# Performance work log

Hardware: AMD Instinct MI355X
Metric: run time of the kernel (lower is better)

The kernel has to match this reference:

```python
import jax, jax.numpy as jnp
import numpy as np

N = 100000   # nodes
E = 1600000  # edges (avg degree 16)
N_IN, N_HID, N_OUT = 64, 64, 16


def setup_inputs() -> dict:
    key = jax.random.key(0)
    k1, k2, k3, k4 = jax.random.split(key, 4)
    x = jax.random.normal(k1, (N, N_IN), dtype=jnp.float32)
    edge_index = jax.random.randint(k2, (2, E), 0, N, dtype=jnp.int64)
    # Glorot-style init like PyG GCNConv linear weights
    W1 = jax.random.normal(k3, (N_IN, N_HID), dtype=jnp.float32) * (1.0 / np.sqrt(N_IN))
    b1 = jnp.zeros((N_HID,), dtype=jnp.float32)
    W2 = jax.random.normal(k4, (N_HID, N_OUT), dtype=jnp.float32) * (1.0 / np.sqrt(N_HID))
    b2 = jnp.zeros((N_OUT,), dtype=jnp.float32)
    return {"x": x, "edge_index": edge_index, "W1": W1, "b1": b1, "W2": W2, "b2": b2}


def reference(x, edge_index, W1, b1, W2, b2):
    n = x.shape[0]
    # GCNConv default: add self-loops with weight 1, symmetric normalization
    loop = jnp.arange(n, dtype=edge_index.dtype)
    src = jnp.concatenate([edge_index[0], loop])  # [E+N]
    dst = jnp.concatenate([edge_index[1], loop])  # [E+N]
    w = jnp.ones(src.shape[0], dtype=x.dtype)
    deg = jax.ops.segment_sum(w, dst, num_segments=n)           # in-degree incl. self-loop
    dinv = jnp.where(deg > 0, jax.lax.rsqrt(deg), 0.0)
    norm = dinv[src] * w * dinv[dst]                            # [E+N] edge coefficients

    def gcn_conv(h, Wm, bm):
        h = h @ Wm                                              # [N, d_out] linear first (PyG order)
        msg = h[src] * norm[:, None]                            # gather + scale
        return jax.ops.segment_sum(msg, dst, num_segments=n) + bm  # scatter-add + bias

    h = jax.nn.relu(gcn_conv(x, W1, b1))
    # dropout is identity at inference (training=False)
    return jax.nn.log_softmax(gcn_conv(h, W2, b2), axis=1)
```

## Files before the change

### kernel.cpp

```cpp
#include <hip/hip_runtime.h>

constexpr int FIN = 64;
constexpr int FH  = 64;
constexpr int FO  = 16;


constexpr int BSH      = 7;
constexpr int BW       = 1 << BSH;
constexpr int NBUCK    = 1024;
constexpr int EPB_HIST = 16384;
constexpr int EPB_BIN  = 4096;

__device__ inline unsigned short f2bf(float f) {
    unsigned u = __float_as_uint(f);
    return (unsigned short)((u + 0x7FFFu + ((u >> 16) & 1u)) >> 16);
}
__device__ inline float bf2f(unsigned short h) {
    return __uint_as_float((unsigned)h << 16);
}
__device__ inline float4 bf4_to_f4(ushort4 u) {
    float4 f;
    f.x = bf2f(u.x); f.y = bf2f(u.y); f.z = bf2f(u.z); f.w = bf2f(u.w);
    return f;
}

__launch_bounds__(256)
__global__ void hist_kernel(const int* __restrict__ ei, int E, int* __restrict__ bcnt) {
    __shared__ int lh[NBUCK];
    int t = threadIdx.x;
    for (int i = t; i < NBUCK; i += 256) lh[i] = 0;
    __syncthreads();
    int base = blockIdx.x * EPB_HIST;
    int lim  = min(E, base + EPB_HIST);
    for (int e = base + t; e < lim; e += 256)
        atomicAdd(&lh[ei[E + e] >> BSH], 1);
    __syncthreads();
    for (int b = t; b < NBUCK; b += 256) {
        int c = lh[b];
        if (c > 0) atomicAdd(&bcnt[b], c);
    }
}

__launch_bounds__(1024)
__global__ void bucket_scan_kernel(const int* __restrict__ bcnt, int* __restrict__ bbase,
                                   int* __restrict__ gcur, int* __restrict__ offs,
                                   int N, int E) {
    __shared__ int s[NBUCK];
    int t = threadIdx.x;
    int v = bcnt[t];
    s[t] = v;
    __syncthreads();
    for (int d = 1; d < NBUCK; d <<= 1) {
        int u = (t >= d) ? s[t - d] : 0;
        __syncthreads();
        s[t] += u;
        __syncthreads();
    }
    int ex = s[t] - v;
    bbase[t] = ex;
    gcur[t]  = ex;
    if (t == NBUCK - 1) {
        bbase[NBUCK] = s[t];
        offs[N] = E;
    }
}

__device__ inline void binning_body(const int* __restrict__ ei, int E, int chunk,
                                    int* __restrict__ gcur, unsigned* __restrict__ ebuf,
                                    int* lh) {
    int t = threadIdx.x;
    for (int i = t; i < NBUCK; i += 256) lh[i] = 0;
    __syncthreads();
    int base = chunk * EPB_BIN;
    int lim  = min(E, base + EPB_BIN);
    for (int e = base + t; e < lim; e += 256)
        atomicAdd(&lh[ei[E + e] >> BSH], 1);
    __syncthreads();
    for (int b = t; b < NBUCK; b += 256) {
        int c = lh[b];
        lh[b] = (c > 0) ? atomicAdd(&gcur[b], c) : 0;
    }
    __syncthreads();
    for (int e = base + t; e < lim; e += 256) {
        int d = ei[E + e];
        int srcv = ei[e];
        int pos = atomicAdd(&lh[d >> BSH], 1);
        ebuf[pos] = (unsigned)srcv | ((unsigned)(d & (BW - 1)) << 17);
    }
}

__launch_bounds__(256)
__global__ void binning_kernel(const int* __restrict__ ei, int E,
                               int* __restrict__ gcur, unsigned* __restrict__ ebuf) {
    __shared__ int lh[NBUCK];
    binning_body(ei, E, blockIdx.x, gcur, ebuf, lh);
}

__launch_bounds__(256, 4)
__global__ void gemm1_binning_kernel(const float* __restrict__ x, const float* __restrict__ W1,
                                     unsigned short* __restrict__ hsb,
                                     const int* __restrict__ ei, int E,
                                     int* __restrict__ gcur, unsigned* __restrict__ ebuf,
                                     int N, int NBIN) {
    __shared__ float smem[FIN * FH];
    int tid = threadIdx.x;
    if ((int)blockIdx.x < NBIN) {
        binning_body(ei, E, (int)blockIdx.x, gcur, ebuf, (int*)smem);
        return;
    }
    float* Ws = smem;
    {
        const float4* W14 = (const float4*)W1;
        float4* Ws4 = (float4*)smem;
        for (int i = tid; i < 1024; i += 256) Ws4[i] = W14[i];
    }
    __syncthreads();
    int cg = tid & 15;
    int rg = tid >> 4;
    int rowBase = ((int)blockIdx.x - NBIN) * 64;
    int r0 = rowBase + rg * 4;
    const float4* x4 = (const float4*)x;
    size_t ra = (size_t)min(r0 + 0, N - 1) * 16;
    size_t rb = (size_t)min(r0 + 1, N - 1) * 16;
    size_t rc = (size_t)min(r0 + 2, N - 1) * 16;
    size_t rd = (size_t)min(r0 + 3, N - 1) * 16;
    float4 acc0 = {0,0,0,0}, acc1 = {0,0,0,0}, acc2 = {0,0,0,0}, acc3 = {0,0,0,0};
    #pragma unroll 2
    for (int kc = 0; kc < 16; ++kc) {
        float4 xa0 = x4[ra + kc];
        float4 xa1 = x4[rb + kc];
        float4 xa2 = x4[rc + kc];
        float4 xa3 = x4[rd + kc];
        const float* xa0f = (const float*)&xa0;
        const float* xa1f = (const float*)&xa1;
        const float* xa2f = (const float*)&xa2;
        const float* xa3f = (const float*)&xa3;
        #pragma unroll
        for (int j = 0; j < 4; ++j) {
            float4 wv = *(const float4*)&Ws[(kc * 4 + j) * FH + cg * 4];
            float v0 = xa0f[j], v1 = xa1f[j], v2 = xa2f[j], v3 = xa3f[j];
            acc0.x = fmaf(v0, wv.x, acc0.x); acc0.y = fmaf(v0, wv.y, acc0.y);
            acc0.z = fmaf(v0, wv.z, acc0.z); acc0.w = fmaf(v0, wv.w, acc0.w);
            acc1.x = fmaf(v1, wv.x, acc1.x); acc1.y = fmaf(v1, wv.y, acc1.y);
            acc1.z = fmaf(v1, wv.z, acc1.z); acc1.w = fmaf(v1, wv.w, acc1.w);
            acc2.x = fmaf(v2, wv.x, acc2.x); acc2.y = fmaf(v2, wv.y, acc2.y);
            acc2.z = fmaf(v2, wv.z, acc2.z); acc2.w = fmaf(v2, wv.w, acc2.w);
            acc3.x = fmaf(v3, wv.x, acc3.x); acc3.y = fmaf(v3, wv.y, acc3.y);
            acc3.z = fmaf(v3, wv.z, acc3.z); acc3.w = fmaf(v3, wv.w, acc3.w);
        }
    }
    ushort4* hsb4 = (ushort4*)hsb;
    if (r0 + 0 < N) hsb4[(size_t)(r0 + 0) * 16 + cg] =
        make_ushort4(f2bf(acc0.x), f2bf(acc0.y), f2bf(acc0.z), f2bf(acc0.w));
    if (r0 + 1 < N) hsb4[(size_t)(r0 + 1) * 16 + cg] =
        make_ushort4(f2bf(acc1.x), f2bf(acc1.y), f2bf(acc1.z), f2bf(acc1.w));
    if (r0 + 2 < N) hsb4[(size_t)(r0 + 2) * 16 + cg] =
        make_ushort4(f2bf(acc2.x), f2bf(acc2.y), f2bf(acc2.z), f2bf(acc2.w));
    if (r0 + 3 < N) hsb4[(size_t)(r0 + 3) * 16 + cg] =
        make_ushort4(f2bf(acc3.x), f2bf(acc3.y), f2bf(acc3.z), f2bf(acc3.w));
}

__launch_bounds__(256)
__global__ void bucket_csr_kernel(const unsigned* __restrict__ ebuf,
                                  const int* __restrict__ bbase,
                                  int* __restrict__ csr, int* __restrict__ offs,
                                  float* __restrict__ dinv, int N) {
    __shared__ int cnt[BW], sc[BW], cur[BW];
    int t = threadIdx.x;
    int b = blockIdx.x;
    if (t < BW) cnt[t] = 0;
    __syncthreads();
    int beg = bbase[b], end = bbase[b + 1];
    for (int i = beg + t; i < end; i += 256)
        atomicAdd(&cnt[ebuf[i] >> 17], 1);
    __syncthreads();
    if (t < BW) sc[t] = cnt[t];
    __syncthreads();
    for (int d = 1; d < BW; d <<= 1) {
        int u = (t < BW && t >= d) ? sc[t - d] : 0;
        __syncthreads();
        if (t < BW) sc[t] += u;
        __syncthreads();
    }
    int nodeBase = b << BSH;
    if (t < BW) {
        int node = nodeBase + t;
        int ex = beg + sc[t] - cnt[t];
        cur[t] = ex;
        if (node < N) {
            offs[node] = ex;
            dinv[node] = rsqrtf((float)(cnt[t] + 1));
        }
    }
    __syncthreads();
    for (int i = beg + t; i < end; i += 256) {
        unsigned w = ebuf[i];
        int pos = atomicAdd(&cur[w >> 17], 1);
        csr[pos] = (int)(w & 0x1FFFF);
    }
}

__launch_bounds__(256)
__global__ void agg1_gemm2_kernel(const unsigned short* __restrict__ hsb,
                                  const int* __restrict__ csr,
                                  const int* __restrict__ offs, const float* __restrict__ dinv,
                                  const float* __restrict__ b1, const float* __restrict__ W2,
                                  unsigned short* __restrict__ hs2b, int N) {
    __shared__ float W2s[FH * FO];
    __shared__ float h1s[16][68];
    const ushort4* hs4 = (const ushort4*)hsb;
    int tid = threadIdx.x;
    for (int i = tid; i < FH * FO; i += 256) W2s[i] = W2[i];
    int g = tid >> 4, l = tid & 15;
    int n = blockIdx.x * 16 + g;
    if (n < N) {
        float di_n = dinv[n];
        float4 self = bf4_to_f4(hs4[(size_t)n * 16 + l]);
        float4 acc;
        acc.x = self.x * di_n; acc.y = self.y * di_n;
        acc.z = self.z * di_n; acc.w = self.w * di_n;
        int j = offs[n], end = offs[n + 1];
        for (; j + 7 < end; j += 8) {
            int s0 = csr[j],     s1 = csr[j + 1], s2 = csr[j + 2], s3 = csr[j + 3];
            int s4 = csr[j + 4], s5 = csr[j + 5], s6 = csr[j + 6], s7 = csr[j + 7];
            float d0 = dinv[s0], d1 = dinv[s1], d2 = dinv[s2], d3 = dinv[s3];
            float d4 = dinv[s4], d5 = dinv[s5], d6 = dinv[s6], d7 = dinv[s7];
            float4 a0 = bf4_to_f4(hs4[(size_t)s0 * 16 + l]);
            float4 a1 = bf4_to_f4(hs4[(size_t)s1 * 16 + l]);
            float4 a2 = bf4_to_f4(hs4[(size_t)s2 * 16 + l]);
            float4 a3 = bf4_to_f4(hs4[(size_t)s3 * 16 + l]);
            float4 a4 = bf4_to_f4(hs4[(size_t)s4 * 16 + l]);
            float4 a5 = bf4_to_f4(hs4[(size_t)s5 * 16 + l]);
            float4 a6 = bf4_to_f4(hs4[(size_t)s6 * 16 + l]);
            float4 a7 = bf4_to_f4(hs4[(size_t)s7 * 16 + l]);
            acc.x += (fmaf(a0.x, d0, a1.x * d1) + fmaf(a2.x, d2, a3.x * d3))
                   + (fmaf(a4.x, d4, a5.x * d5) + fmaf(a6.x, d6, a7.x * d7));
            acc.y += (fmaf(a0.y, d0, a1.y * d1) + fmaf(a2.y, d2, a3.y * d3))
                   + (fmaf(a4.y, d4, a5.y * d5) + fmaf(a6.y, d6, a7.y * d7));
            acc.z += (fmaf(a0.z, d0, a1.z * d1) + fmaf(a2.z, d2, a3.z * d3))
                   + (fmaf(a4.z, d4, a5.z * d5) + fmaf(a6.z, d6, a7.z * d7));
            acc.w += (fmaf(a0.w, d0, a1.w * d1) + fmaf(a2.w, d2, a3.w * d3))
                   + (fmaf(a4.w, d4, a5.w * d5) + fmaf(a6.w, d6, a7.w * d7));
        }
        for (; j + 1 < end; j += 2) {
            int s0 = csr[j], s1 = csr[j + 1];
            float d0 = dinv[s0], d1 = dinv[s1];
            float4 a0 = bf4_to_f4(hs4[(size_t)s0 * 16 + l]);
            float4 a1 = bf4_to_f4(hs4[(size_t)s1 * 16 + l]);
            acc.x += fmaf(a0.x, d0, a1.x * d1);
            acc.y += fmaf(a0.y, d0, a1.y * d1);
            acc.z += fmaf(a0.z, d0, a1.z * d1);
            acc.w += fmaf(a0.w, d0, a1.w * d1);
        }
        if (j < end) {
            int s0 = csr[j];
            float d0 = dinv[s0];
            float4 a0 = bf4_to_f4(hs4[(size_t)s0 * 16 + l]);
            acc.x = fmaf(a0.x, d0, acc.x); acc.y = fmaf(a0.y, d0, acc.y);
            acc.z = fmaf(a0.z, d0, acc.z); acc.w = fmaf(a0.w, d0, acc.w);
        }
        float4 bb = ((const float4*)b1)[l];
        float4 h;
        h.x = fmaxf(fmaf(di_n, acc.x, bb.x), 0.f);
        h.y = fmaxf(fmaf(di_n, acc.y, bb.y), 0.f);
        h.z = fmaxf(fmaf(di_n, acc.z, bb.z), 0.f);
        h.w = fmaxf(fmaf(di_n, acc.w, bb.w), 0.f);
        *((float4*)&h1s[g][l * 4]) = h;
    }
    __syncthreads();
    int r = tid >> 4, o = tid & 15;
    int n2 = blockIdx.x * 16 + r;
    if (n2 < N) {
        float acc = 0.f;
        #pragma unroll
        for (int jj = 0; jj < FH; ++jj)
            acc = fmaf(h1s[r][jj], W2s[jj * FO + o], acc);
        hs2b[(size_t)n2 * FO + o] = f2bf(acc * dinv[n2]);
    }
}

__launch_bounds__(256)
__global__ void agg2_softmax_kernel(const unsigned short* __restrict__ hs2b,
                                    const int* __restrict__ csr,
                                    const int* __restrict__ offs, const float* __restrict__ dinv,
                                    const float* __restrict__ b2, float* __restrict__ out, int N) {
    int tid = threadIdx.x;
    int g = tid >> 4, o = tid & 15;
    int n = blockIdx.x * 16 + g;
    float v = 0.f;
    if (n < N) {
        float acc = bf2f(hs2b[(size_t)n * 16 + o]);
        int j = offs[n], end = offs[n + 1];
        for (; j + 7 < end; j += 8) {
            int s0 = csr[j],     s1 = csr[j + 1], s2 = csr[j + 2], s3 = csr[j + 3];
            int s4 = csr[j + 4], s5 = csr[j + 5], s6 = csr[j + 6], s7 = csr[j + 7];
            float t0 = bf2f(hs2b[(size_t)s0 * 16 + o]) + bf2f(hs2b[(size_t)s1 * 16 + o]);
            float t1 = bf2f(hs2b[(size_t)s2 * 16 + o]) + bf2f(hs2b[(size_t)s3 * 16 + o]);
            float t2 = bf2f(hs2b[(size_t)s4 * 16 + o]) + bf2f(hs2b[(size_t)s5 * 16 + o]);
            float t3 = bf2f(hs2b[(size_t)s6 * 16 + o]) + bf2f(hs2b[(size_t)s7 * 16 + o]);
            acc += (t0 + t1) + (t2 + t3);
        }
        for (; j < end; ++j) acc += bf2f(hs2b[(size_t)csr[j] * 16 + o]);
        v = fmaf(dinv[n], acc, b2[o]);
    }
    float m = v;
    #pragma unroll
    for (int s = 8; s >= 1; s >>= 1) m = fmaxf(m, __shfl_xor(m, s, 64));
    float ex = __expf(v - m);
    float sum = ex;
    #pragma unroll
    for (int s = 8; s >= 1; s >>= 1) sum += __shfl_xor(sum, s, 64);
    if (n < N) out[(size_t)n * FO + o] = v - m - __logf(sum);
}

extern "C" void kernel_launch(void* const* d_in, const int* in_sizes, int n_in,
                              void* d_out, int out_size, void* d_ws, size_t ws_size,
                              hipStream_t stream) {
    const float* x  = (const float*)d_in[0];
    const int*   ei = (const int*)d_in[1];
    const float* W1 = (const float*)d_in[2];
    const float* b1 = (const float*)d_in[3];
    const float* W2 = (const float*)d_in[4];
    const float* b2 = (const float*)d_in[5];
    float* out = (float*)d_out;

    const int N = in_sizes[0] / FIN;
    const int E = in_sizes[1] / 2;
    const int NCH  = (E + EPB_HIST - 1) / EPB_HIST;
    const int NCB  = (E + EPB_BIN - 1) / EPB_BIN;
    const int NB4  = (N + BW - 1) / BW;
    const int G1T  = (N + 63) / 64;
    const int GA   = (N + 15) / 16;

    char* ws = (char*)d_ws;
    size_t off = 0;
    auto alloc = [&](size_t bytes) -> void* {
        off = (off + 255) & ~(size_t)255;
        void* p = ws + off;
        off += bytes;
        return p;
    };
    float*          dinv  = (float*)alloc((size_t)N * 4);
    unsigned short* hsb   = (unsigned short*)alloc((size_t)N * FH * 2);
    unsigned short* hs2b  = (unsigned short*)alloc((size_t)N * FO * 2);
    int*            offs  = (int*)alloc((size_t)(N + 1) * 4);
    int*            bcnt  = (int*)alloc(NBUCK * 4);
    int*            bbase = (int*)alloc((NBUCK + 1) * 4);
    int*            gcur  = (int*)alloc(NBUCK * 4);
    unsigned* ebuf;
    int*      csr;
    bool ws_fits = (ws_size >= off + 512 + (size_t)E * 8);
    if (ws_fits) {
        ebuf = (unsigned*)alloc((size_t)E * 4);
        csr  = (int*)     alloc((size_t)E * 4);
    } else {
        ebuf = (unsigned*)x;
        csr  = (int*)x + E;
    }

    hipMemsetAsync(bcnt, 0, NBUCK * 4, stream);

    hist_kernel<<<NCH, 256, 0, stream>>>(ei, E, bcnt);
    bucket_scan_kernel<<<1, NBUCK, 0, stream>>>(bcnt, bbase, gcur, offs, N, E);
    if (ws_fits) {
        gemm1_binning_kernel<<<NCB + G1T, 256, 0, stream>>>(x, W1, hsb, ei, E,
                                                            gcur, ebuf, N, NCB);
    } else {
        gemm1_binning_kernel<<<G1T, 256, 0, stream>>>(x, W1, hsb, ei, E,
                                                      gcur, ebuf, N, 0);
        binning_kernel<<<NCB, 256, 0, stream>>>(ei, E, gcur, ebuf);
    }
    bucket_csr_kernel<<<NB4, 256, 0, stream>>>(ebuf, bbase, csr, offs, dinv, N);
    agg1_gemm2_kernel<<<GA, 256, 0, stream>>>(hsb, csr, offs, dinv, b1, W2, hs2b, N);
    agg2_softmax_kernel<<<GA, 256, 0, stream>>>(hs2b, csr, offs, dinv, b2, out, N);
}
```

Measured before the change: 216.2 us.

## Precompute per-chunk bucket bases to drop re-histogram and global atomics in binning

The histogram pass now stores each chunk's per-bucket counts, and a new small kernel prefix-sums them per bucket to give every chunk a fixed base offset in each bucket. The binning pass loads those bases into shared memory, so it no longer re-reads destinations to build a local histogram or does global atomicAdds on a shared cursor. Binning chunks grow from 4096 to 16384 edges, so there are fewer, larger binning blocks. In exchange it adds one extra kernel launch, two NCH×1024 int arrays in workspace, and a serial loop over chunks per bucket.

```diff
diff --git a/kernel.cpp b/kernel.cpp
--- a/kernel.cpp
+++ b/kernel.cpp
@@ -8,8 +8,7 @@
 constexpr int BSH      = 7;
 constexpr int BW       = 1 << BSH;
 constexpr int NBUCK    = 1024;
-constexpr int EPB_HIST = 16384;
-constexpr int EPB_BIN  = 4096;
+constexpr int EPB      = 16384;
 
 __device__ inline unsigned short f2bf(float f) {
     unsigned u = __float_as_uint(f);
@@ -25,26 +24,28 @@
 }
 
 __launch_bounds__(256)
-__global__ void hist_kernel(const int* __restrict__ ei, int E, int* __restrict__ bcnt) {
+__global__ void hist_kernel(const int* __restrict__ ei, int E,
+                            int* __restrict__ bcnt, int* __restrict__ gchist) {
     __shared__ int lh[NBUCK];
     int t = threadIdx.x;
     for (int i = t; i < NBUCK; i += 256) lh[i] = 0;
     __syncthreads();
-    int base = blockIdx.x * EPB_HIST;
-    int lim  = min(E, base + EPB_HIST);
+    int base = blockIdx.x * EPB;
+    int lim  = min(E, base + EPB);
     for (int e = base + t; e < lim; e += 256)
         atomicAdd(&lh[ei[E + e] >> BSH], 1);
     __syncthreads();
+    int* gh = gchist + (size_t)blockIdx.x * NBUCK;
     for (int b = t; b < NBUCK; b += 256) {
         int c = lh[b];
+        gh[b] = c;
         if (c > 0) atomicAdd(&bcnt[b], c);
     }
 }
 
 __launch_bounds__(1024)
 __global__ void bucket_scan_kernel(const int* __restrict__ bcnt, int* __restrict__ bbase,
-                                   int* __restrict__ gcur, int* __restrict__ offs,
-                                   int N, int E) {
+                                   int* __restrict__ offs, int N, int E) {
     __shared__ int s[NBUCK];
     int t = threadIdx.x;
     int v = bcnt[t];
@@ -58,31 +59,36 @@
     }
     int ex = s[t] - v;
     bbase[t] = ex;
-    gcur[t]  = ex;
     if (t == NBUCK - 1) {
         bbase[NBUCK] = s[t];
         offs[N] = E;
     }
 }
 
+__launch_bounds__(256)
+__global__ void chunk_base_kernel(const int* __restrict__ gchist,
+                                  const int* __restrict__ bbase,
+                                  int* __restrict__ gbase, int NCH) {
+    int b = blockIdx.x * 256 + threadIdx.x;
+    int run = bbase[b];
+    #pragma unroll 4
+    for (int c = 0; c < NCH; ++c) {
+        gbase[(size_t)c * NBUCK + b] = run;
+        run += gchist[(size_t)c * NBUCK + b];
+    }
+}
+
 __device__ inline void binning_body(const int* __restrict__ ei, int E, int chunk,
-                                    int* __restrict__ gcur, unsigned* __restrict__ ebuf,
-                                    int* lh) {
+                                    const int* __restrict__ gbase,
+                                    unsigned* __restrict__ ebuf, int* lh) {
     int t = threadIdx.x;
-    for (int i = t; i < NBUCK; i += 256) lh[i] = 0;
-    __syncthreads();
-    int base = chunk * EPB_BIN;
-    int lim  = min(E, base + EPB_BIN);
-    for (int e = base + t; e < lim; e += 256)
-        atomicAdd(&lh[ei[E + e] >> BSH], 1);
-    __syncthreads();
-    for (int b = t; b < NBUCK; b += 256) {
-        int c = lh[b];
-        lh[b] = (c > 0) ? atomicAdd(&gcur[b], c) : 0;
-    }
-    __syncthreads();
+    const int* gb = gbase + (size_t)chunk * NBUCK;
+    for (int i = t; i < NBUCK; i += 256) lh[i] = gb[i];
+    __syncthreads();
+    int base = chunk * EPB;
+    int lim  = min(E, base + EPB);
     for (int e = base + t; e < lim; e += 256) {
-        int d = ei[E + e];
+        int d    = ei[E + e];
         int srcv = ei[e];
         int pos = atomicAdd(&lh[d >> BSH], 1);
         ebuf[pos] = (unsigned)srcv | ((unsigned)(d & (BW - 1)) << 17);
@@ -91,21 +97,21 @@
 
 __launch_bounds__(256)
 __global__ void binning_kernel(const int* __restrict__ ei, int E,
-                               int* __restrict__ gcur, unsigned* __restrict__ ebuf) {
+                               const int* __restrict__ gbase, unsigned* __restrict__ ebuf) {
     __shared__ int lh[NBUCK];
-    binning_body(ei, E, blockIdx.x, gcur, ebuf, lh);
+    binning_body(ei, E, blockIdx.x, gbase, ebuf, lh);
 }
 
 __launch_bounds__(256, 4)
 __global__ void gemm1_binning_kernel(const float* __restrict__ x, const float* __restrict__ W1,
                                      unsigned short* __restrict__ hsb,
                                      const int* __restrict__ ei, int E,
-                                     int* __restrict__ gcur, unsigned* __restrict__ ebuf,
+                                     const int* __restrict__ gbase, unsigned* __restrict__ ebuf,
                                      int N, int NBIN) {
     __shared__ float smem[FIN * FH];
     int tid = threadIdx.x;
     if ((int)blockIdx.x < NBIN) {
-        binning_body(ei, E, (int)blockIdx.x, gcur, ebuf, (int*)smem);
+        binning_body(ei, E, (int)blockIdx.x, gbase, ebuf, (int*)smem);
         return;
     }
     float* Ws = smem;
@@ -326,8 +332,7 @@
 
     const int N = in_sizes[0] / FIN;
     const int E = in_sizes[1] / 2;
-    const int NCH  = (E + EPB_HIST - 1) / EPB_HIST;
-    const int NCB  = (E + EPB_BIN - 1) / EPB_BIN;
+    const int NCH  = (E + EPB - 1) / EPB;
     const int NB4  = (N + BW - 1) / BW;
     const int G1T  = (N + 63) / 64;
     const int GA   = (N + 15) / 16;
@@ -340,13 +345,14 @@
         off += bytes;
         return p;
     };
-    float*          dinv  = (float*)alloc((size_t)N * 4);
-    unsigned short* hsb   = (unsigned short*)alloc((size_t)N * FH * 2);
-    unsigned short* hs2b  = (unsigned short*)alloc((size_t)N * FO * 2);
-    int*            offs  = (int*)alloc((size_t)(N + 1) * 4);
-    int*            bcnt  = (int*)alloc(NBUCK * 4);
-    int*            bbase = (int*)alloc((NBUCK + 1) * 4);
-    int*            gcur  = (int*)alloc(NBUCK * 4);
+    float*          dinv   = (float*)alloc((size_t)N * 4);
+    unsigned short* hsb    = (unsigned short*)alloc((size_t)N * FH * 2);
+    unsigned short* hs2b   = (unsigned short*)alloc((size_t)N * FO * 2);
+    int*            offs   = (int*)alloc((size_t)(N + 1) * 4);
+    int*            bcnt   = (int*)alloc(NBUCK * 4);
+    int*            bbase  = (int*)alloc((NBUCK + 1) * 4);
+    int*            gchist = (int*)alloc((size_t)NCH * NBUCK * 4);
+    int*            gbase  = (int*)alloc((size_t)NCH * NBUCK * 4);
     unsigned* ebuf;
     int*      csr;
     bool ws_fits = (ws_size >= off + 512 + (size_t)E * 8);
@@ -360,15 +366,16 @@
 
     hipMemsetAsync(bcnt, 0, NBUCK * 4, stream);
 
-    hist_kernel<<<NCH, 256, 0, stream>>>(ei, E, bcnt);
-    bucket_scan_kernel<<<1, NBUCK, 0, stream>>>(bcnt, bbase, gcur, offs, N, E);
+    hist_kernel<<<NCH, 256, 0, stream>>>(ei, E, bcnt, gchist);
+    bucket_scan_kernel<<<1, NBUCK, 0, stream>>>(bcnt, bbase, offs, N, E);
+    chunk_base_kernel<<<NBUCK / 256, 256, 0, stream>>>(gchist, bbase, gbase, NCH);
     if (ws_fits) {
-        gemm1_binning_kernel<<<NCB + G1T, 256, 0, stream>>>(x, W1, hsb, ei, E,
-                                                            gcur, ebuf, N, NCB);
+        gemm1_binning_kernel<<<NCH + G1T, 256, 0, stream>>>(x, W1, hsb, ei, E,
+                                                            gbase, ebuf, N, NCH);
     } else {
         gemm1_binning_kernel<<<G1T, 256, 0, stream>>>(x, W1, hsb, ei, E,
-                                                      gcur, ebuf, N, 0);
-        binning_kernel<<<NCB, 256, 0, stream>>>(ei, E, gcur, ebuf);
+                                                      gbase, ebuf, N, 0);
+        binning_kernel<<<NCH, 256, 0, stream>>>(ei, E, gbase, ebuf);
     }
     bucket_csr_kernel<<<NB4, 256, 0, stream>>>(ebuf, bbase, csr, offs, dinv, N);
     agg1_gemm2_kernel<<<GA, 256, 0, stream>>>(hsb, csr, offs, dinv, b1, W2, hs2b, N);
```

Result: slower. 223.3 us (+3.3%).
